# Performance work log

Measured on AMD Instinct MI355X. Metric: run time of the kernel, lower is better.

The kernel has to match this reference:

```python
import jax, jax.numpy as jnp
import numpy as np

INPUT_DIM = 16
NUM_MFS = 4
NUM_RULES = 1024
NUM_CLASSES = 10
BATCH = 4096


def setup_inputs() -> dict:
    key = jax.random.key(0)
    k1, k2, k3, k4, k5 = jax.random.split(key, 5)
    x = jax.random.normal(k1, (BATCH, INPUT_DIM), dtype=jnp.float32)
    centers = jax.random.normal(k2, (INPUT_DIM, NUM_MFS), dtype=jnp.float32)
    # widths must be positive (used as std of gaussian)
    widths = jax.random.uniform(k3, (INPUT_DIM, NUM_MFS), dtype=jnp.float32, minval=0.2, maxval=1.2)
    consequents = jax.random.normal(k4, (NUM_RULES, INPUT_DIM + 1, NUM_CLASSES), dtype=jnp.float32)
    rule_idx = jax.random.randint(k5, (INPUT_DIM, NUM_RULES), 0, NUM_MFS, dtype=jnp.int32)
    return {"x": x, "centers": centers, "widths": widths,
            "consequents": consequents, "rule_idx": rule_idx}


def reference(x, centers, widths, consequents, rule_idx):
    B, D = x.shape
    # Gaussian membership functions: [B, D, M]
    mfs = jnp.exp(-((x[:, :, None] - centers[None]) ** 2) / (2.0 * widths[None] ** 2) + 1e-9)
    # Gather rule-specific memberships: [B, D, R]
    d_idx = jnp.arange(D)[:, None]  # [D, 1] broadcasts with rule_idx [D, R]
    rule_mfs = mfs[:, d_idx, rule_idx]
    # Firing strengths (product over input dims) and normalization: [B, R]
    firing = jnp.prod(rule_mfs, axis=1)
    norm_fs = firing / (jnp.sum(firing, axis=1, keepdims=True) + 1e-9)
    # Extended input with bias column: [B, D+1]
    x_ext = jnp.concatenate([x, jnp.ones((B, 1), dtype=x.dtype)], axis=1)
    # phi = norm_fs[:, :, None] * x_ext[:, None, :]; y = phi_flat @ beta_flat
    # expressed as a single contraction (same math, phi is detached w.r.t. x_ext)
    y_hat = jnp.einsum('br,bi,ric->bc', norm_fs, jax.lax.stop_gradient(x_ext), consequents)
    return y_hat, norm_fs, x_ext
```

## Files before the change

### kernel.cpp

```cpp
#include <hip/hip_runtime.h>

#define B 4096
#define D 16
#define R 1024
#define NC 10
#define IC 170
#define NT 11
#define NP 176
#define KC 64
#define KSPLIT 4
#define RPB (R / KSPLIT)
#define BT 16
#define BSTR 72
#define GSP 192

typedef __attribute__((ext_vector_type(8))) short short8;
typedef __attribute__((ext_vector_type(4))) float f32x4;

__device__ __forceinline__ unsigned short f2bf(float f) {
    unsigned u = __float_as_uint(f);
    return (unsigned short)((u + 0x7fffu + ((u >> 16) & 1u)) >> 16);
}

__global__ void pack_rules(const int* __restrict__ rule_idx, unsigned* __restrict__ packed) {
    int r = blockIdx.x * 256 + threadIdx.x;
    unsigned bits = 0;
#pragma unroll
    for (int d = 0; d < D; ++d)
        bits |= (((unsigned)rule_idx[d * R + r]) & 3u) << (2 * d);
    packed[r] = bits;
}

__global__ __launch_bounds__(256) void convert_b(const float* __restrict__ cons,
                                                 unsigned short* __restrict__ Bsw) {
    int t = blockIdx.x * 256 + threadIdx.x;
    int row = t >> 10;
    int k   = t & 1023;
    float v = (row < IC) ? cons[(size_t)k * IC + row] : 0.0f;
    Bsw[t] = f2bf(v);
}

__global__ __launch_bounds__(256) void firing_kernel(
    const float* __restrict__ x, const float* __restrict__ centers,
    const float* __restrict__ widths, const unsigned* __restrict__ packed,
    float* __restrict__ out_norm, float* __restrict__ out_xext,
    float* __restrict__ out_y)
{
    __shared__ float s_z[64];
    __shared__ float s_z2[8][16];
    __shared__ float s_z4[4 * 256];
    __shared__ float s_red[8];
    const int b = blockIdx.x, tid = threadIdx.x;

    if (b < (B * NC) / 256) out_y[b * 256 + tid] = 0.0f;

    if (tid < 64) {
        int d = tid >> 2;
        float xv = x[b * D + d];
        float c = centers[tid], w = widths[tid];
        float diff = xv - c;
        s_z[tid] = 1e-9f - diff * diff / (2.0f * w * w);
    }
    if (tid < 17) out_xext[b * 17 + tid] = (tid < 16) ? x[b * D + tid] : 1.0f;
    __syncthreads();
    if (tid < 128) {
        int p = tid >> 4, i = tid & 15;
        s_z2[p][i] = s_z[p * 8 + (i & 3)] + s_z[p * 8 + 4 + ((i >> 2) & 3)];
    }
    __syncthreads();
#pragma unroll
    for (int q = 0; q < 4; ++q)
        s_z4[q * 256 + tid] = s_z2[2 * q][tid & 15] + s_z2[2 * q + 1][(tid >> 4) & 15];
    __syncthreads();

    float f[4], lsum = 0.0f;
#pragma unroll
    for (int j = 0; j < 4; ++j) {
        unsigned w = packed[tid + 256 * j];
        float s = s_z4[w & 255] + s_z4[256 + ((w >> 8) & 255)]
                + s_z4[512 + ((w >> 16) & 255)] + s_z4[768 + (w >> 24)];
        f[j] = __expf(s);
        lsum += f[j];
    }
#pragma unroll
    for (int off = 1; off < 64; off <<= 1) lsum += __shfl_xor(lsum, off, 64);
    const int lane = tid & 63, wid = tid >> 6;
    if (lane == 0) s_red[wid] = lsum;
    __syncthreads();
    if (tid == 0) {
        float tot = s_red[0] + s_red[1] + s_red[2] + s_red[3] + 1e-9f;
        s_red[4] = 1.0f / tot;
    }
    __syncthreads();
    const float inv = s_red[4];
#pragma unroll
    for (int j = 0; j < 4; ++j)
        out_norm[(size_t)b * R + tid + 256 * j] = f[j] * inv;
}

__global__ __launch_bounds__(256, 4) void yhat_kernel(
    const float* __restrict__ norm, const unsigned short* __restrict__ Bsw,
    const float* __restrict__ x, float* __restrict__ out_y)
{
    __shared__ unsigned short Bs[NT * 16 * BSTR];
    __shared__ unsigned short As[BT * BSTR];
    __shared__ float xe[BT * 17];

    const int tid = threadIdx.x;
    const int mt = blockIdx.x & 255;
    const int ks = blockIdx.x >> 8;
    const int bl0 = mt * BT;
    const int r_base = ks * RPB;

    for (int t = tid; t < BT * 17; t += 256) {
        int bl = t / 17, i = t - bl * 17;
        xe[t] = (i < 16) ? x[(size_t)(bl0 + bl) * D + i] : 1.0f;
    }

    const int lane = tid & 63, wv = tid >> 6;
    const int m_ = lane & 15, q_ = lane >> 4;
    const int nt0 = wv * 3;
    const int ntn = (wv == 3) ? 2 : 3;

    f32x4 acc[3];
    const f32x4 zf = {0.f, 0.f, 0.f, 0.f};
    acc[0] = zf; acc[1] = zf; acc[2] = zf;

    for (int c0 = 0; c0 < RPB; c0 += KC) {
        const int kabs = r_base + c0;
        __syncthreads();
        for (int t = tid; t < NP * 8; t += 256) {
            int row = t >> 3, seg = t & 7;
            *(short8*)&Bs[row * BSTR + seg * 8] =
                *(const short8*)&Bsw[row * R + kabs + seg * 8];
        }
        {
            int row = tid >> 4, c4 = tid & 15;
            float4 v = *(const float4*)&norm[(size_t)(bl0 + row) * R + kabs + c4 * 4];
            ushort4 o;
            o.x = f2bf(v.x); o.y = f2bf(v.y); o.z = f2bf(v.z); o.w = f2bf(v.w);
            *(ushort4*)&As[row * BSTR + c4 * 4] = o;
        }
        __syncthreads();
#pragma unroll
        for (int kh = 0; kh < 2; ++kh) {
            short8 a = *(const short8*)&As[m_ * BSTR + kh * 32 + q_ * 8];
#pragma unroll
            for (int j = 0; j < 3; ++j) {
                if (j < ntn) {
                    int nt = nt0 + j;
                    short8 bfrag = *(const short8*)&Bs[(nt * 16 + m_) * BSTR + kh * 32 + q_ * 8];
                    acc[j] = __builtin_amdgcn_mfma_f32_16x16x32_bf16(a, bfrag, acc[j], 0, 0, 0);
                }
            }
        }
    }

    __syncthreads();
    float* Gs = (float*)Bs;
#pragma unroll
    for (int j = 0; j < 3; ++j) {
        if (j < ntn) {
            int nt = nt0 + j;
#pragma unroll
            for (int r = 0; r < 4; ++r)
                Gs[(q_ * 4 + r) * GSP + nt * 16 + m_] = acc[j][r];
        }
    }
    __syncthreads();
    if (tid < BT * NC) {
        int bl = tid / NC, c = tid - bl * NC;
        float y = 0.0f;
#pragma unroll
        for (int i = 0; i < 17; ++i)
            y += xe[bl * 17 + i] * Gs[bl * GSP + i * NC + c];
        atomicAdd(&out_y[(size_t)(bl0 + bl) * NC + c], y);
    }
}

extern "C" void kernel_launch(void* const* d_in, const int* in_sizes, int n_in,
                              void* d_out, int out_size, void* d_ws, size_t ws_size,
                              hipStream_t stream) {
    const float* x        = (const float*)d_in[0];
    const float* centers  = (const float*)d_in[1];
    const float* widths   = (const float*)d_in[2];
    const float* cons     = (const float*)d_in[3];
    const int*   rule_idx = (const int*)d_in[4];

    float* out      = (float*)d_out;
    float* out_y    = out;
    float* out_norm = out + (size_t)B * NC;
    float* out_xext = out + (size_t)B * NC + (size_t)B * R;

    unsigned* packed     = (unsigned*)d_ws;
    unsigned short* Bsw  = (unsigned short*)((char*)d_ws + 4096);

    pack_rules<<<R / 256, 256, 0, stream>>>(rule_idx, packed);
    convert_b<<<(NP * R) / 256, 256, 0, stream>>>(cons, Bsw);
    firing_kernel<<<B, 256, 0, stream>>>(x, centers, widths, packed,
                                         out_norm, out_xext, out_y);
    yhat_kernel<<<(B / BT) * KSPLIT, 256, 0, stream>>>(out_norm, Bsw, x, out_y);
}
```

Baseline: 94.17 us.

## Merge prep kernels and load MFMA operands directly from global memory

Merges pack_rules and convert_b into one prep kernel, which also zero-fills out_y and writes x_ext, so there are fewer launches and firing_kernel does less side work. The consequent transpose now goes through an LDS tile, so both the global reads and the writes are coalesced. In yhat_kernel the LDS staging and per-chunk barriers are gone: each lane loads its A fragment (with on-the-fly bf16 conversion) and its B fragment straight from global memory into MFMA registers, in a fully unrolled loop. The trade-off is that B rows are re-read from global or cache by every wave with uncoalesced 16-byte accesses instead of being shared through LDS.

```diff
diff --git a/kernel.cpp b/kernel.cpp
--- a/kernel.cpp
+++ b/kernel.cpp
@@ -7,12 +7,11 @@
 #define IC 170
 #define NT 11
 #define NP 176
-#define KC 64
 #define KSPLIT 4
 #define RPB (R / KSPLIT)
 #define BT 16
-#define BSTR 72
 #define GSP 192
+#define TSTR 72
 
 typedef __attribute__((ext_vector_type(8))) short short8;
 typedef __attribute__((ext_vector_type(4))) float f32x4;
@@ -22,29 +21,51 @@
     return (unsigned short)((u + 0x7fffu + ((u >> 16) & 1u)) >> 16);
 }
 
-__global__ void pack_rules(const int* __restrict__ rule_idx, unsigned* __restrict__ packed) {
-    int r = blockIdx.x * 256 + threadIdx.x;
-    unsigned bits = 0;
-#pragma unroll
-    for (int d = 0; d < D; ++d)
-        bits |= (((unsigned)rule_idx[d * R + r]) & 3u) << (2 * d);
-    packed[r] = bits;
-}
-
-__global__ __launch_bounds__(256) void convert_b(const float* __restrict__ cons,
-                                                 unsigned short* __restrict__ Bsw) {
-    int t = blockIdx.x * 256 + threadIdx.x;
-    int row = t >> 10;
-    int k   = t & 1023;
-    float v = (row < IC) ? cons[(size_t)k * IC + row] : 0.0f;
-    Bsw[t] = f2bf(v);
+__global__ __launch_bounds__(256) void prep_kernel(
+    const float* __restrict__ cons, const int* __restrict__ rule_idx,
+    const float* __restrict__ x, unsigned* __restrict__ packed,
+    unsigned short* __restrict__ Bsw, float* __restrict__ out_y,
+    float* __restrict__ out_xext)
+{
+    __shared__ unsigned short T[NP * TSTR];
+    const int blk = blockIdx.x, tid = threadIdx.x;
+
+    if (blk < 16) {
+        const int k0 = blk * 64;
+        for (int t = tid; t < 64 * IC; t += 256) {
+            int k = t / IC, c = t - k * IC;
+            T[c * TSTR + k] = f2bf(cons[(size_t)(k0 + k) * IC + c]);
+        }
+        for (int t = tid; t < (NP - IC) * 64; t += 256) {
+            int c = IC + t / 64, k = t & 63;
+            T[c * TSTR + k] = 0;
+        }
+        __syncthreads();
+        for (int t = tid; t < NP * 8; t += 256) {
+            int row = t >> 3, seg = t & 7;
+            *(short8*)&Bsw[(size_t)row * R + k0 + seg * 8] =
+                *(const short8*)&T[row * TSTR + seg * 8];
+        }
+    } else if (blk < 20) {
+        int r = (blk - 16) * 256 + tid;
+        unsigned bits = 0;
+#pragma unroll
+        for (int d = 0; d < D; ++d)
+            bits |= (((unsigned)rule_idx[d * R + r]) & 3u) << (2 * d);
+        packed[r] = bits;
+    } else if (blk < 180) {
+        out_y[(blk - 20) * 256 + tid] = 0.0f;
+    } else {
+        int t = (blk - 180) * 256 + tid;
+        int b = t / 17, i = t - b * 17;
+        out_xext[t] = (i < 16) ? x[b * D + i] : 1.0f;
+    }
 }
 
 __global__ __launch_bounds__(256) void firing_kernel(
     const float* __restrict__ x, const float* __restrict__ centers,
     const float* __restrict__ widths, const unsigned* __restrict__ packed,
-    float* __restrict__ out_norm, float* __restrict__ out_xext,
-    float* __restrict__ out_y)
+    float* __restrict__ out_norm)
 {
     __shared__ float s_z[64];
     __shared__ float s_z2[8][16];
@@ -52,8 +73,6 @@
     __shared__ float s_red[8];
     const int b = blockIdx.x, tid = threadIdx.x;
 
-    if (b < (B * NC) / 256) out_y[b * 256 + tid] = 0.0f;
-
     if (tid < 64) {
         int d = tid >> 2;
         float xv = x[b * D + d];
@@ -61,7 +80,6 @@
         float diff = xv - c;
         s_z[tid] = 1e-9f - diff * diff / (2.0f * w * w);
     }
-    if (tid < 17) out_xext[b * 17 + tid] = (tid < 16) ? x[b * D + tid] : 1.0f;
     __syncthreads();
     if (tid < 128) {
         int p = tid >> 4, i = tid & 15;
@@ -102,8 +120,7 @@
     const float* __restrict__ norm, const unsigned short* __restrict__ Bsw,
     const float* __restrict__ x, float* __restrict__ out_y)
 {
-    __shared__ unsigned short Bs[NT * 16 * BSTR];
-    __shared__ unsigned short As[BT * BSTR];
+    __shared__ float Gs[BT * GSP];
     __shared__ float xe[BT * 17];
 
     const int tid = threadIdx.x;
@@ -126,38 +143,29 @@
     const f32x4 zf = {0.f, 0.f, 0.f, 0.f};
     acc[0] = zf; acc[1] = zf; acc[2] = zf;
 
-    for (int c0 = 0; c0 < RPB; c0 += KC) {
-        const int kabs = r_base + c0;
-        __syncthreads();
-        for (int t = tid; t < NP * 8; t += 256) {
-            int row = t >> 3, seg = t & 7;
-            *(short8*)&Bs[row * BSTR + seg * 8] =
-                *(const short8*)&Bsw[row * R + kabs + seg * 8];
-        }
-        {
-            int row = tid >> 4, c4 = tid & 15;
-            float4 v = *(const float4*)&norm[(size_t)(bl0 + row) * R + kabs + c4 * 4];
-            ushort4 o;
-            o.x = f2bf(v.x); o.y = f2bf(v.y); o.z = f2bf(v.z); o.w = f2bf(v.w);
-            *(ushort4*)&As[row * BSTR + c4 * 4] = o;
-        }
-        __syncthreads();
-#pragma unroll
-        for (int kh = 0; kh < 2; ++kh) {
-            short8 a = *(const short8*)&As[m_ * BSTR + kh * 32 + q_ * 8];
-#pragma unroll
-            for (int j = 0; j < 3; ++j) {
-                if (j < ntn) {
-                    int nt = nt0 + j;
-                    short8 bfrag = *(const short8*)&Bs[(nt * 16 + m_) * BSTR + kh * 32 + q_ * 8];
-                    acc[j] = __builtin_amdgcn_mfma_f32_16x16x32_bf16(a, bfrag, acc[j], 0, 0, 0);
-                }
+    const float* aptr = &norm[(size_t)(bl0 + m_) * R + r_base + q_ * 8];
+    const unsigned short* bptr = &Bsw[(size_t)r_base + q_ * 8];
+
+#pragma unroll
+    for (int kk = 0; kk < RPB; kk += 32) {
+        float4 a0 = *(const float4*)(aptr + kk);
+        float4 a1 = *(const float4*)(aptr + kk + 4);
+        short8 a;
+        a[0] = (short)f2bf(a0.x); a[1] = (short)f2bf(a0.y);
+        a[2] = (short)f2bf(a0.z); a[3] = (short)f2bf(a0.w);
+        a[4] = (short)f2bf(a1.x); a[5] = (short)f2bf(a1.y);
+        a[6] = (short)f2bf(a1.z); a[7] = (short)f2bf(a1.w);
+#pragma unroll
+        for (int j = 0; j < 3; ++j) {
+            if (j < ntn) {
+                int row = (nt0 + j) * 16 + m_;
+                short8 bf = *(const short8*)&bptr[(size_t)row * R + kk];
+                acc[j] = __builtin_amdgcn_mfma_f32_16x16x32_bf16(a, bf, acc[j], 0, 0, 0);
             }
         }
     }
 
     __syncthreads();
-    float* Gs = (float*)Bs;
 #pragma unroll
     for (int j = 0; j < 3; ++j) {
         if (j < ntn) {
@@ -195,9 +203,7 @@
     unsigned* packed     = (unsigned*)d_ws;
     unsigned short* Bsw  = (unsigned short*)((char*)d_ws + 4096);
 
-    pack_rules<<<R / 256, 256, 0, stream>>>(rule_idx, packed);
-    convert_b<<<(NP * R) / 256, 256, 0, stream>>>(cons, Bsw);
-    firing_kernel<<<B, 256, 0, stream>>>(x, centers, widths, packed,
-                                         out_norm, out_xext, out_y);
+    prep_kernel<<<452, 256, 0, stream>>>(cons, rule_idx, x, packed, Bsw, out_y, out_xext);
+    firing_kernel<<<B, 256, 0, stream>>>(x, centers, widths, packed, out_norm);
     yhat_kernel<<<(B / BT) * KSPLIT, 256, 0, stream>>>(out_norm, Bsw, x, out_y);
 }
```

New measurement: 102.3 us. 8.6% more time.
